# Optimization experiments

Hardware: AMD Instinct MI355X
Metric: run time of the kernel (lower is better)

## Reference

```python
import jax, jax.numpy as jnp
import numpy as np

B, L, E = 4, 1024, 1024
H, D = 16, 64          # num_heads, head_dim
HID = H * D            # hidden_dim == 1024
R = 4                  # nrels


def setup_inputs() -> dict:
    key = jax.random.key(0)
    ks = jax.random.split(key, 8)
    query = jax.random.normal(ks[0], (B, L, E), dtype=jnp.float32)
    rels = jax.random.uniform(ks[1], (B, L, L, R), dtype=jnp.float32)
    attn_mask = jax.random.normal(ks[2], (B, L, L), dtype=jnp.float32)
    key_padding_mask = jax.random.bernoulli(ks[3], 0.9, (B, L, L))
    # xavier-ish init for linear weights
    proj_w = jax.random.normal(ks[4], (4 * HID, E), dtype=jnp.float32) * (2.0 / (4 * HID + E)) ** 0.5
    proj_b = jnp.zeros((4 * HID,), dtype=jnp.float32)
    out_w = jax.random.normal(ks[5], (E, HID), dtype=jnp.float32) * (2.0 / (E + HID)) ** 0.5
    out_b = jnp.zeros((E,), dtype=jnp.float32)
    rels_bias = jax.random.uniform(ks[6], (R, H), dtype=jnp.float32, minval=-0.1, maxval=0.1)
    return {"query": query, "rels": rels, "attn_mask": attn_mask,
            "key_padding_mask": key_padding_mask, "proj_w": proj_w, "proj_b": proj_b,
            "out_w": out_w, "out_b": out_b, "rels_bias": rels_bias}


def reference(query, rels, attn_mask, key_padding_mask, proj_w, proj_b, out_w, out_b, rels_bias):
    b, l, _ = query.shape
    # fused QKVG projection
    qkvg = query @ proj_w.T + proj_b                       # [b, l, 4*HID]
    q, k, v, g = jnp.split(qkvg, 4, axis=-1)
    q = q.reshape(b, l, H, D)
    k = k.reshape(b, l, H, D)
    v = v.reshape(b, l, H, D)
    g = g.reshape(b, l, H, D)
    scores = jnp.einsum('bihd,bjhd->bijh', q, k)
    scores = scores + jnp.einsum('bijr,rh->bijh', rels, rels_bias)
    scores = scores * (D ** -0.5)
    # NOTE: log_softmax over the HEADS axis (dim=-1), as in the source,
    # then additive log-domain mask over keys, then exp.
    w = jnp.exp(jax.nn.log_softmax(scores, axis=-1) + attn_mask[:, :, :, None])
    w = jnp.where(key_padding_mask[:, :, :, None], w, 0.0)
    attn_out = jnp.einsum('bijh,bjhd->bihd', w, jnp.tanh(v))
    gated = attn_out * jax.nn.sigmoid(g)                   # [b, l, H, D]
    out = gated.reshape(b, l, HID) @ out_w.T + out_b       # [b, l, E]
    return (out, w)
```

## Files before the change

kernel.cpp:

```cpp
#include <hip/hip_runtime.h>

typedef unsigned short u16;
using bf16x8 = __attribute__((ext_vector_type(8))) short;
using f32x4  = __attribute__((ext_vector_type(4))) float;

__device__ __forceinline__ u16 f2bf(float f) {
  unsigned u = __builtin_bit_cast(unsigned, f);
  u += 0x7fffu + ((u >> 16) & 1u);
  return (u16)(u >> 16);
}
__device__ __forceinline__ float bf2f(u16 h) {
  unsigned u = ((unsigned)h) << 16;
  return __builtin_bit_cast(float, u);
}
__device__ __forceinline__ float f16f(unsigned bits) {
  return (float)__builtin_bit_cast(_Float16, (unsigned short)(bits & 0xffffu));
}
__device__ __forceinline__ float fast_rcp(float x){ return __builtin_amdgcn_rcpf(x); }
__device__ __forceinline__ float tanh_fast(float x){
  float ax = fabsf(x);
  float e = __expf(-2.f*ax);
  float t = (1.f - e) * fast_rcp(1.f + e);
  return copysignf(t, x);
}
__device__ __forceinline__ float sigmoid_fast(float x){
  return fast_rcp(1.f + __expf(-x));
}

__global__ __launch_bounds__(256) void cvt_bf16(const float* __restrict__ src,
                                                u16* __restrict__ dst, int n){
  int i = (blockIdx.x * 256 + threadIdx.x) * 8;
  if (i >= n) return;
  float4 a = *(const float4*)(src + i);
  float4 b = *(const float4*)(src + i + 4);
  uint4 u;
  u.x = (unsigned)f2bf(a.x) | ((unsigned)f2bf(a.y) << 16);
  u.y = (unsigned)f2bf(a.z) | ((unsigned)f2bf(a.w) << 16);
  u.z = (unsigned)f2bf(b.x) | ((unsigned)f2bf(b.y) << 16);
  u.w = (unsigned)f2bf(b.z) | ((unsigned)f2bf(b.w) << 16);
  *(uint4*)(dst + i) = u;
}

template<int EPI>
__global__ __launch_bounds__(256, 2) void gemm_bt(
    const u16* __restrict__ A, const u16* __restrict__ B, const float* __restrict__ bias,
    u16* __restrict__ oq, u16* __restrict__ ok, u16* __restrict__ ov, u16* __restrict__ og,
    float* __restrict__ outp, int K)
{
  __shared__ u16 a_lds[4*128*8];
  __shared__ u16 b_lds[4*128*8];
  const int tid  = threadIdx.x;
  const int lane = tid & 63;
  const int wv   = tid >> 6;
  const int wr   = wv >> 1, wc = wv & 1;
  const int col  = lane & 15, quad = lane >> 4;
  const int m0   = blockIdx.y * 128, n0 = blockIdx.x * 128;
  f32x4 acc[4][4] = {};
  for (int k0 = 0; k0 < K; k0 += 32) {
    __syncthreads();
    #pragma unroll
    for (int s = 0; s < 2; s++) {
      int cid = tid + 256*s;
      int row = cid >> 2, qk = cid & 3;
      *(bf16x8*)(&a_lds[(qk*128+row)*8]) = *(const bf16x8*)(A + (m0+row)*K + k0 + qk*8);
      *(bf16x8*)(&b_lds[(qk*128+row)*8]) = *(const bf16x8*)(B + (n0+row)*K + k0 + qk*8);
    }
    __syncthreads();
    bf16x8 af[4], bfr[4];
    #pragma unroll
    for (int mi=0;mi<4;mi++) af[mi]  = *(const bf16x8*)(&a_lds[(quad*128 + wr*64 + mi*16 + col)*8]);
    #pragma unroll
    for (int ni=0;ni<4;ni++) bfr[ni] = *(const bf16x8*)(&b_lds[(quad*128 + wc*64 + ni*16 + col)*8]);
    #pragma unroll
    for (int mi=0;mi<4;mi++)
      #pragma unroll
      for (int ni=0;ni<4;ni++)
        acc[mi][ni] = __builtin_amdgcn_mfma_f32_16x16x32_bf16(af[mi], bfr[ni], acc[mi][ni], 0, 0, 0);
  }
  #pragma unroll
  for (int mi=0;mi<4;mi++) {
    #pragma unroll
    for (int ni=0;ni<4;ni++) {
      #pragma unroll
      for (int r=0;r<4;r++) {
        const int m = m0 + wr*64 + mi*16 + quad*4 + r;
        const int n = n0 + wc*64 + ni*16 + col;
        const float val = acc[mi][ni][r] + bias[n];
        if (EPI == 0) {
          const int idx = m*1024 + (n & 1023);
          const int quarter = n0 >> 10;
          if (quarter == 0)      oq[idx] = f2bf(val);
          else if (quarter == 1) ok[idx] = f2bf(val);
          else if (quarter == 2) ov[idx] = f2bf(tanh_fast(val));
          else                   og[idx] = f2bf(sigmoid_fast(val));
        } else {
          outp[m*1024 + n] = val;
        }
      }
    }
  }
}

__global__ __launch_bounds__(256) void vtrans(const u16* __restrict__ vin, u16* __restrict__ vout){
  __shared__ u16 tile[64][68];
  const int bh = blockIdx.y;
  const int b = bh >> 4, h = bh & 15;
  const int i0 = blockIdx.x * 64;
  const int t = threadIdx.x;
  #pragma unroll
  for (int s=0;s<4;s++){
    int idx = t + 256*s;
    int ti = idx >> 4;
    int d4 = (idx & 15) * 4;
    uint2 v = *(const uint2*)(vin + ((size_t)((b*1024 + i0 + ti)*16 + h))*64 + d4);
    tile[ti][d4+0] = (u16)(v.x);
    tile[ti][d4+1] = (u16)(v.x >> 16);
    tile[ti][d4+2] = (u16)(v.y);
    tile[ti][d4+3] = (u16)(v.y >> 16);
  }
  __syncthreads();
  #pragma unroll
  for (int s=0;s<4;s++){
    int idx = t + 256*s;
    int d  = idx >> 4;
    int t4 = (idx & 15) * 4;
    uint2 o;
    o.x = (unsigned)tile[t4+0][d] | ((unsigned)tile[t4+1][d] << 16);
    o.y = (unsigned)tile[t4+2][d] | ((unsigned)tile[t4+3][d] << 16);
    *(uint2*)(vout + ((size_t)((b*16 + h)*64 + d))*1024 + i0 + t4) = o;
  }
}

__global__ __launch_bounds__(256, 3) void attn_kernel(
    const u16* __restrict__ qb, const u16* __restrict__ kb,
    const u16* __restrict__ vt,
    const float* __restrict__ rels, const float* __restrict__ amask,
    const int* __restrict__ kpm, const float* __restrict__ rbias,
    float* __restrict__ wout,
    u16* __restrict__ o0, u16* __restrict__ o1, u16* __restrict__ o2)
{
  __shared__ u16 w_lds[16*16*72];
  const int bid = blockIdx.x;
  const int b  = (bid >> 1) & 3;
  const int it = (bid & 1) | ((bid >> 3) << 1);
  const int i0 = it << 4;
  const int js = blockIdx.y;
  const int t0 = js*5 + (js > 0);
  const int t1 = t0 + (js == 0 ? 6 : 5);
  const int tid = threadIdx.x;
  const int lane = tid & 63;
  const int wv  = tid >> 6;
  const int col = lane & 15, quad = lane >> 4;

  float rbv[4][16];
  #pragma unroll
  for (int r=0;r<4;r++)
    #pragma unroll
    for (int h=0;h<16;h++)
      rbv[r][h] = rbias[r*16+h];

  f32x4 Oa[4][4] = {};

  for (int t = t0; t < t1; t++) {
    const int j0b = t << 6;
    const int j0  = j0b + (wv << 4);
    f32x4 sc[16] = {};
    #pragma unroll
    for (int h=0; h<16; h++) {
      #pragma unroll
      for (int c=0; c<2; c++) {
        bf16x8 aq = *(const bf16x8*)(qb + (size_t)(b*1024 + i0 + col)*1024 + h*64 + c*32 + quad*8);
        bf16x8 bk = *(const bf16x8*)(kb + (size_t)(b*1024 + j0 + col)*1024 + h*64 + c*32 + quad*8);
        sc[h] = __builtin_amdgcn_mfma_f32_16x16x32_bf16(aq, bk, sc[h], 0, 0, 0);
      }
    }
    #pragma unroll
    for (int r=0; r<4; r++) {
      const int i = i0 + quad*4 + r;
      const int j = j0 + col;
      const int pij = (b*1024 + i)*1024 + j;
      const float4 rl = *(const float4*)(rels + (size_t)pij*4);
      const float mk = amask[pij];
      const int   pd = kpm[pij];
      float p[16];
      float mx = -1e30f;
      #pragma unroll
      for (int h=0;h<16;h++) {
        float s = sc[h][r];
        s = fmaf(rl.x, rbv[0][h], s);
        s = fmaf(rl.y, rbv[1][h], s);
        s = fmaf(rl.z, rbv[2][h], s);
        s = fmaf(rl.w, rbv[3][h], s);
        s *= 0.125f;
        p[h] = s;
        mx = fmaxf(mx, s);
      }
      float S = 0.f;
      #pragma unroll
      for (int h=0;h<16;h++) { p[h] = __expf(p[h] - mx); S += p[h]; }
      const float scl = pd ? (__expf(mk) * fast_rcp(S)) : 0.f;
      #pragma unroll
      for (int h=0;h<16;h++) p[h] *= scl;
      float4* wp = (float4*)(wout + (size_t)pij*16);
      wp[0] = make_float4(p[0], p[1], p[2], p[3]);
      wp[1] = make_float4(p[4], p[5], p[6], p[7]);
      wp[2] = make_float4(p[8], p[9], p[10], p[11]);
      wp[3] = make_float4(p[12],p[13],p[14],p[15]);
      #pragma unroll
      for (int h=0;h<16;h++)
        w_lds[(h*16 + quad*4 + r)*72 + (wv<<4) + col] = f2bf(p[h]);
    }
    __syncthreads();
    #pragma unroll
    for (int hh=0; hh<4; hh++) {
      const int h = (wv<<2) + hh;
      #pragma unroll
      for (int c2=0; c2<2; c2++) {
        bf16x8 aw = *(const bf16x8*)(&w_lds[(h*16 + col)*72 + c2*32 + quad*8]);
        #pragma unroll
        for (int dt=0; dt<4; dt++) {
          bf16x8 bv = *(const bf16x8*)(vt + (size_t)((b*16 + h)*64 + dt*16 + col)*1024 + j0b + c2*32 + quad*8);
          Oa[hh][dt] = __builtin_amdgcn_mfma_f32_16x16x32_bf16(aw, bv, Oa[hh][dt], 0, 0, 0);
        }
      }
    }
    __syncthreads();
  }
  u16* op = (js == 0) ? o0 : ((js == 1) ? o1 : o2);
  #pragma unroll
  for (int hh=0; hh<4; hh++) {
    const int h = (wv<<2) + hh;
    #pragma unroll
    for (int dt=0; dt<4; dt++) {
      #pragma unroll
      for (int r=0; r<4; r++) {
        const int i = i0 + quad*4 + r;
        const int d = dt*16 + col;
        const int idx = ((b*1024 + i)*16 + h)*64 + d;
        _Float16 hv = (_Float16)Oa[hh][dt][r];
        op[idx] = __builtin_bit_cast(unsigned short, hv);
      }
    }
  }
}

__global__ __launch_bounds__(256) void reduce_gate(
    const u16* o0, const u16* __restrict__ o1, const u16* __restrict__ o2,
    const u16* __restrict__ sg, u16* gated)
{
  const int i = (blockIdx.x * 256 + threadIdx.x) * 8;
  uint4 a = *(const uint4*)(o0 + i);
  uint4 b = *(const uint4*)(o1 + i);
  uint4 c = *(const uint4*)(o2 + i);
  uint4 s = *(const uint4*)(sg + i);
  const unsigned* ap = (const unsigned*)&a;
  const unsigned* bp = (const unsigned*)&b;
  const unsigned* cp = (const unsigned*)&c;
  const unsigned* sp = (const unsigned*)&s;
  uint4 r;
  unsigned* rp = (unsigned*)&r;
  #pragma unroll
  for (int k=0;k<4;k++){
    float f0 = f16f(ap[k]) + f16f(bp[k]) + f16f(cp[k]);
    float f1 = f16f(ap[k]>>16) + f16f(bp[k]>>16) + f16f(cp[k]>>16);
    f0 *= bf2f((u16)(sp[k] & 0xffffu));
    f1 *= bf2f((u16)(sp[k] >> 16));
    rp[k] = (unsigned)f2bf(f0) | ((unsigned)f2bf(f1) << 16);
  }
  *(uint4*)(gated + i) = r;
}

extern "C" void kernel_launch(void* const* d_in, const int* in_sizes, int n_in,
                              void* d_out, int out_size, void* d_ws, size_t ws_size,
                              hipStream_t stream) {
  const float* query  = (const float*)d_in[0];
  const float* rels   = (const float*)d_in[1];
  const float* amask  = (const float*)d_in[2];
  const int*   kpm    = (const int*)d_in[3];
  const float* proj_w = (const float*)d_in[4];
  const float* proj_b = (const float*)d_in[5];
  const float* out_w  = (const float*)d_in[6];
  const float* out_b  = (const float*)d_in[7];
  const float* rbias  = (const float*)d_in[8];

  float* out  = (float*)d_out;
  float* wout = out + (size_t)4*1024*1024;

  char* ws = (char*)d_ws;
  u16* q_b   = (u16*)(ws + ((size_t) 0 << 20));
  u16* k_b   = (u16*)(ws + ((size_t) 8 << 20));
  u16* sg_b  = (u16*)(ws + ((size_t)16 << 20));
  u16* vth   = (u16*)(ws + ((size_t)24 << 20));
  u16* vt    = (u16*)(ws + ((size_t)32 << 20));
  u16* qryb  = (u16*)(ws + ((size_t)40 << 20));
  u16* pwb   = (u16*)(ws + ((size_t)48 << 20));
  u16* owb   = (u16*)(ws + ((size_t)56 << 20));
  u16* o0 = qryb;
  u16* o1 = pwb;
  u16* o2 = vth;
  u16* gated = o0;

  cvt_bf16<<<2048, 256, 0, stream>>>(query,  qryb, 4*1024*1024);
  cvt_bf16<<<2048, 256, 0, stream>>>(proj_w, pwb,  4*1024*1024);
  cvt_bf16<<< 512, 256, 0, stream>>>(out_w,  owb,  1024*1024);

  gemm_bt<0><<<dim3(32,32), 256, 0, stream>>>(qryb, pwb, proj_b,
                                              q_b, k_b, vth, sg_b, nullptr, 1024);
  vtrans<<<dim3(16,64), 256, 0, stream>>>(vth, vt);
  attn_kernel<<<dim3(256,3), 256, 0, stream>>>(q_b, k_b, vt,
                                               rels, amask, kpm, rbias, wout,
                                               o0, o1, o2);
  reduce_gate<<<2048, 256, 0, stream>>>(o0, o1, o2, sg_b, gated);
  gemm_bt<1><<<dim3(8,32), 256, 0, stream>>>(gated, owb, out_b,
                                             nullptr, nullptr, nullptr, nullptr, out, 1024);
}
```

Measured before the change: 759.3 us.

## Split attention over four key chunks, prefetch per-tile inputs, use nontemporal weight stores

The attention kernel now splits the key axis into four equal chunks of four tiles instead of three uneven ones. Launch bounds go from three to four blocks per SM, and the reduce kernel sums four partial outputs, with the fourth partial buffer placed in the output region that the final GEMM overwrites later. The rels, mask and padding loads are hoisted ahead of the score MFMAs so their latency overlaps compute. The large attention-weight output is written with nontemporal stores so it does not pollute the cache. The aims are more parallelism and hidden memory latency, at the cost of register pressure and an extra partial buffer to read.

```diff
diff --git a/kernel.cpp b/kernel.cpp
--- a/kernel.cpp
+++ b/kernel.cpp
@@ -131,13 +131,14 @@
   }
 }
 
-__global__ __launch_bounds__(256, 3) void attn_kernel(
+__global__ __launch_bounds__(256, 4) void attn_kernel(
     const u16* __restrict__ qb, const u16* __restrict__ kb,
     const u16* __restrict__ vt,
     const float* __restrict__ rels, const float* __restrict__ amask,
     const int* __restrict__ kpm, const float* __restrict__ rbias,
     float* __restrict__ wout,
-    u16* __restrict__ o0, u16* __restrict__ o1, u16* __restrict__ o2)
+    u16* __restrict__ o0, u16* __restrict__ o1,
+    u16* __restrict__ o2, u16* __restrict__ o3)
 {
   __shared__ u16 w_lds[16*16*72];
   const int bid = blockIdx.x;
@@ -145,8 +146,8 @@
   const int it = (bid & 1) | ((bid >> 3) << 1);
   const int i0 = it << 4;
   const int js = blockIdx.y;
-  const int t0 = js*5 + (js > 0);
-  const int t1 = t0 + (js == 0 ? 6 : 5);
+  const int t0 = js << 2;
+  const int t1 = t0 + 4;
   const int tid = threadIdx.x;
   const int lane = tid & 63;
   const int wv  = tid >> 6;
@@ -164,6 +165,14 @@
   for (int t = t0; t < t1; t++) {
     const int j0b = t << 6;
     const int j0  = j0b + (wv << 4);
+    float4 rl4[4]; float mk4[4]; int pd4[4];
+    #pragma unroll
+    for (int r=0; r<4; r++) {
+      const int pij = (b*1024 + i0 + quad*4 + r)*1024 + j0 + col;
+      rl4[r] = *(const float4*)(rels + (size_t)pij*4);
+      mk4[r] = amask[pij];
+      pd4[r] = kpm[pij];
+    }
     f32x4 sc[16] = {};
     #pragma unroll
     for (int h=0; h<16; h++) {
@@ -179,9 +188,7 @@
       const int i = i0 + quad*4 + r;
       const int j = j0 + col;
       const int pij = (b*1024 + i)*1024 + j;
-      const float4 rl = *(const float4*)(rels + (size_t)pij*4);
-      const float mk = amask[pij];
-      const int   pd = kpm[pij];
+      const float4 rl = rl4[r];
       float p[16];
       float mx = -1e30f;
       #pragma unroll
@@ -198,14 +205,18 @@
       float S = 0.f;
       #pragma unroll
       for (int h=0;h<16;h++) { p[h] = __expf(p[h] - mx); S += p[h]; }
-      const float scl = pd ? (__expf(mk) * fast_rcp(S)) : 0.f;
+      const float scl = pd4[r] ? (__expf(mk4[r]) * fast_rcp(S)) : 0.f;
       #pragma unroll
       for (int h=0;h<16;h++) p[h] *= scl;
-      float4* wp = (float4*)(wout + (size_t)pij*16);
-      wp[0] = make_float4(p[0], p[1], p[2], p[3]);
-      wp[1] = make_float4(p[4], p[5], p[6], p[7]);
-      wp[2] = make_float4(p[8], p[9], p[10], p[11]);
-      wp[3] = make_float4(p[12],p[13],p[14],p[15]);
+      f32x4* wp = (f32x4*)(wout + (size_t)pij*16);
+      f32x4 w0 = { p[0],  p[1],  p[2],  p[3]  };
+      f32x4 w1 = { p[4],  p[5],  p[6],  p[7]  };
+      f32x4 w2 = { p[8],  p[9],  p[10], p[11] };
+      f32x4 w3 = { p[12], p[13], p[14], p[15] };
+      __builtin_nontemporal_store(w0, wp+0);
+      __builtin_nontemporal_store(w1, wp+1);
+      __builtin_nontemporal_store(w2, wp+2);
+      __builtin_nontemporal_store(w3, wp+3);
       #pragma unroll
       for (int h=0;h<16;h++)
         w_lds[(h*16 + quad*4 + r)*72 + (wv<<4) + col] = f2bf(p[h]);
@@ -226,7 +237,7 @@
     }
     __syncthreads();
   }
-  u16* op = (js == 0) ? o0 : ((js == 1) ? o1 : o2);
+  u16* op = (js == 0) ? o0 : ((js == 1) ? o1 : ((js == 2) ? o2 : o3));
   #pragma unroll
   for (int hh=0; hh<4; hh++) {
     const int h = (wv<<2) + hh;
@@ -246,23 +257,26 @@
 
 __global__ __launch_bounds__(256) void reduce_gate(
     const u16* o0, const u16* __restrict__ o1, const u16* __restrict__ o2,
+    const u16* __restrict__ o3,
     const u16* __restrict__ sg, u16* gated)
 {
   const int i = (blockIdx.x * 256 + threadIdx.x) * 8;
   uint4 a = *(const uint4*)(o0 + i);
   uint4 b = *(const uint4*)(o1 + i);
   uint4 c = *(const uint4*)(o2 + i);
+  uint4 d = *(const uint4*)(o3 + i);
   uint4 s = *(const uint4*)(sg + i);
   const unsigned* ap = (const unsigned*)&a;
   const unsigned* bp = (const unsigned*)&b;
   const unsigned* cp = (const unsigned*)&c;
+  const unsigned* dp = (const unsigned*)&d;
   const unsigned* sp = (const unsigned*)&s;
   uint4 r;
   unsigned* rp = (unsigned*)&r;
   #pragma unroll
   for (int k=0;k<4;k++){
-    float f0 = f16f(ap[k]) + f16f(bp[k]) + f16f(cp[k]);
-    float f1 = f16f(ap[k]>>16) + f16f(bp[k]>>16) + f16f(cp[k]>>16);
+    float f0 = (f16f(ap[k])     + f16f(bp[k]))     + (f16f(cp[k])     + f16f(dp[k]));
+    float f1 = (f16f(ap[k]>>16) + f16f(bp[k]>>16)) + (f16f(cp[k]>>16) + f16f(dp[k]>>16));
     f0 *= bf2f((u16)(sp[k] & 0xffffu));
     f1 *= bf2f((u16)(sp[k] >> 16));
     rp[k] = (unsigned)f2bf(f0) | ((unsigned)f2bf(f1) << 16);
@@ -298,6 +312,7 @@
   u16* o0 = qryb;
   u16* o1 = pwb;
   u16* o2 = vth;
+  u16* o3 = (u16*)out;
   u16* gated = o0;
 
   cvt_bf16<<<2048, 256, 0, stream>>>(query,  qryb, 4*1024*1024);
@@ -307,10 +322,10 @@
   gemm_bt<0><<<dim3(32,32), 256, 0, stream>>>(qryb, pwb, proj_b,
                                               q_b, k_b, vth, sg_b, nullptr, 1024);
   vtrans<<<dim3(16,64), 256, 0, stream>>>(vth, vt);
-  attn_kernel<<<dim3(256,3), 256, 0, stream>>>(q_b, k_b, vt,
+  attn_kernel<<<dim3(256,4), 256, 0, stream>>>(q_b, k_b, vt,
                                                rels, amask, kpm, rbias, wout,
-                                               o0, o1, o2);
-  reduce_gate<<<2048, 256, 0, stream>>>(o0, o1, o2, sg_b, gated);
+                                               o0, o1, o2, o3);
+  reduce_gate<<<2048, 256, 0, stream>>>(o0, o1, o2, o3, sg_b, gated);
   gemm_bt<1><<<dim3(8,32), 256, 0, stream>>>(gated, owb, out_b,
                                              nullptr, nullptr, nullptr, nullptr, out, 1024);
 }
```

Measured after the change: 852.6 us. +12.3%, slower.

## Coalesce attention weight stores via LDS staging and pack permuted head outputs

Applied to the files above, without the earlier changes.

The attention kernel now stages each wave's 16x16x16 probability block in shared memory with an XOR swizzle. It then writes the w output as fully contiguous nontemporal float4 rows instead of scattered 64-byte stores per lane. The per-head output is stored as packed 4-element fp16 vectors in a permuted d order. The sigmoid gate and the out_w bf16 copy use the same permutation so the final GEMM stays consistent. rels, mask and padding loads are hoisted ahead of the QK MFMAs to overlap latency, at the cost of 16KB extra LDS per block, which may lower occupancy.

```diff
diff --git a/kernel.cpp b/kernel.cpp
--- a/kernel.cpp
+++ b/kernel.cpp
@@ -15,6 +15,10 @@
 }
 __device__ __forceinline__ float f16f(unsigned bits) {
   return (float)__builtin_bit_cast(_Float16, (unsigned short)(bits & 0xffffu));
+}
+__device__ __forceinline__ u16 f2h(float f) {
+  _Float16 h = (_Float16)f;
+  return __builtin_bit_cast(unsigned short, h);
 }
 __device__ __forceinline__ float fast_rcp(float x){ return __builtin_amdgcn_rcpf(x); }
 __device__ __forceinline__ float tanh_fast(float x){
@@ -25,6 +29,10 @@
 }
 __device__ __forceinline__ float sigmoid_fast(float x){
   return fast_rcp(1.f + __expf(-x));
+}
+
+__device__ __forceinline__ int kperm(int k) {
+  return (k & ~63) | ((k & 15) << 2) | ((k >> 4) & 3);
 }
 
 __global__ __launch_bounds__(256) void cvt_bf16(const float* __restrict__ src,
@@ -39,6 +47,20 @@
   u.z = (unsigned)f2bf(b.x) | ((unsigned)f2bf(b.y) << 16);
   u.w = (unsigned)f2bf(b.z) | ((unsigned)f2bf(b.w) << 16);
   *(uint4*)(dst + i) = u;
+}
+
+__global__ __launch_bounds__(256) void cvt_owb_perm(const float* __restrict__ src,
+                                                    u16* __restrict__ dst){
+  const int t = blockIdx.x * 256 + threadIdx.x;
+  const int n = t >> 8;
+  const int g = t & 255;
+  const int h = g >> 4;
+  const int c = g & 15;
+  const float* s = src + n*1024 + h*64 + c;
+  uint2 o;
+  o.x = (unsigned)f2bf(s[0])  | ((unsigned)f2bf(s[16]) << 16);
+  o.y = (unsigned)f2bf(s[32]) | ((unsigned)f2bf(s[48]) << 16);
+  *(uint2*)(dst + n*1024 + g*4) = o;
 }
 
 template<int EPI>
@@ -92,7 +114,9 @@
           if (quarter == 0)      oq[idx] = f2bf(val);
           else if (quarter == 1) ok[idx] = f2bf(val);
           else if (quarter == 2) ov[idx] = f2bf(tanh_fast(val));
-          else                   og[idx] = f2bf(sigmoid_fast(val));
+          else {
+            og[m*1024 + kperm(n & 1023)] = f2bf(sigmoid_fast(val));
+          }
         } else {
           outp[m*1024 + n] = val;
         }
@@ -140,6 +164,7 @@
     u16* __restrict__ o0, u16* __restrict__ o1, u16* __restrict__ o2)
 {
   __shared__ u16 w_lds[16*16*72];
+  __shared__ float stageF[4][1024];
   const int bid = blockIdx.x;
   const int b  = (bid >> 1) & 3;
   const int it = (bid & 1) | ((bid >> 3) << 1);
@@ -164,6 +189,14 @@
   for (int t = t0; t < t1; t++) {
     const int j0b = t << 6;
     const int j0  = j0b + (wv << 4);
+    float4 rl4[4]; float mk4[4]; int pd4[4];
+    #pragma unroll
+    for (int r=0; r<4; r++) {
+      const int pij = (b*1024 + i0 + quad*4 + r)*1024 + j0 + col;
+      rl4[r] = *(const float4*)(rels + (size_t)pij*4);
+      mk4[r] = amask[pij];
+      pd4[r] = kpm[pij];
+    }
     f32x4 sc[16] = {};
     #pragma unroll
     for (int h=0; h<16; h++) {
@@ -176,12 +209,7 @@
     }
     #pragma unroll
     for (int r=0; r<4; r++) {
-      const int i = i0 + quad*4 + r;
-      const int j = j0 + col;
-      const int pij = (b*1024 + i)*1024 + j;
-      const float4 rl = *(const float4*)(rels + (size_t)pij*4);
-      const float mk = amask[pij];
-      const int   pd = kpm[pij];
+      const float4 rl = rl4[r];
       float p[16];
       float mx = -1e30f;
       #pragma unroll
@@ -198,17 +226,27 @@
       float S = 0.f;
       #pragma unroll
       for (int h=0;h<16;h++) { p[h] = __expf(p[h] - mx); S += p[h]; }
-      const float scl = pd ? (__expf(mk) * fast_rcp(S)) : 0.f;
+      const float scl = pd4[r] ? (__expf(mk4[r]) * fast_rcp(S)) : 0.f;
       #pragma unroll
       for (int h=0;h<16;h++) p[h] *= scl;
-      float4* wp = (float4*)(wout + (size_t)pij*16);
-      wp[0] = make_float4(p[0], p[1], p[2], p[3]);
-      wp[1] = make_float4(p[4], p[5], p[6], p[7]);
-      wp[2] = make_float4(p[8], p[9], p[10], p[11]);
-      wp[3] = make_float4(p[12],p[13],p[14],p[15]);
+      #pragma unroll
+      for (int hg=0; hg<4; hg++) {
+        const int ph = hg ^ ((col + quad) & 3);
+        f32x4 v4 = { p[4*hg+0], p[4*hg+1], p[4*hg+2], p[4*hg+3] };
+        *(f32x4*)&stageF[wv][quad*256 + col*16 + ph*4] = v4;
+      }
       #pragma unroll
       for (int h=0;h<16;h++)
         w_lds[(h*16 + quad*4 + r)*72 + (wv<<4) + col] = f2bf(p[h]);
+      asm volatile("s_waitcnt lgkmcnt(0)" ::: "memory");
+      const int rcol = lane >> 2, rhg = lane & 3;
+      #pragma unroll
+      for (int qt=0; qt<4; qt++) {
+        const int ph = rhg ^ ((rcol + qt) & 3);
+        f32x4 w4 = *(const f32x4*)&stageF[wv][qt*256 + rcol*16 + ph*4];
+        float* dst = wout + ((size_t)((b*1024 + i0 + qt*4 + r)*1024 + j0b + (wv<<4)))*16 + lane*4;
+        __builtin_nontemporal_store(w4, (f32x4*)dst);
+      }
     }
     __syncthreads();
     #pragma unroll
@@ -231,15 +269,12 @@
   for (int hh=0; hh<4; hh++) {
     const int h = (wv<<2) + hh;
     #pragma unroll
-    for (int dt=0; dt<4; dt++) {
-      #pragma unroll
-      for (int r=0; r<4; r++) {
-        const int i = i0 + quad*4 + r;
-        const int d = dt*16 + col;
-        const int idx = ((b*1024 + i)*16 + h)*64 + d;
-        _Float16 hv = (_Float16)Oa[hh][dt][r];
-        op[idx] = __builtin_bit_cast(unsigned short, hv);
-      }
+    for (int r=0; r<4; r++) {
+      const int i = i0 + quad*4 + r;
+      uint2 pk;
+      pk.x = (unsigned)f2h(Oa[hh][0][r]) | ((unsigned)f2h(Oa[hh][1][r]) << 16);
+      pk.y = (unsigned)f2h(Oa[hh][2][r]) | ((unsigned)f2h(Oa[hh][3][r]) << 16);
+      *(uint2*)(op + ((size_t)((b*1024 + i)*16 + h))*64 + col*4) = pk;
     }
   }
 }
@@ -302,7 +337,7 @@
 
   cvt_bf16<<<2048, 256, 0, stream>>>(query,  qryb, 4*1024*1024);
   cvt_bf16<<<2048, 256, 0, stream>>>(proj_w, pwb,  4*1024*1024);
-  cvt_bf16<<< 512, 256, 0, stream>>>(out_w,  owb,  1024*1024);
+  cvt_owb_perm<<<1024, 256, 0, stream>>>(out_w, owb);
 
   gemm_bt<0><<<dim3(32,32), 256, 0, stream>>>(qryb, pwb, proj_b,
                                               q_b, k_b, vth, sg_b, nullptr, 1024);
```

New measurement: 703.9 us. -7.3%, faster.
